# Kernel tuning notes

Measured on AMD Instinct MI355X. Metric: run time of the kernel, lower is better.

Reference implementation:

```python
import jax, jax.numpy as jnp
import numpy as np

HIDDEN = 768
NUM_LABELS = 25


def setup_inputs() -> dict:
    key = jax.random.key(0)
    k1, k2, k3, k4, k5 = jax.random.split(key, 5)
    B, H, S, E = 2, 12, 256, 64
    attention_probs = jax.random.uniform(k1, (B, H, S, S), dtype=jnp.float32)
    value_attentions = jax.random.normal(k2, (B, H, S, E), dtype=jnp.float32)
    relative_positions = jax.random.normal(k3, (B, S, S, H * E), dtype=jnp.float32)
    # nn.Linear(hidden_size, num_labels): weight [L, hidden], bias [L]
    bound = 1.0 / np.sqrt(HIDDEN)
    W = jax.random.uniform(k4, (NUM_LABELS, HIDDEN), dtype=jnp.float32, minval=-bound, maxval=bound)
    b = jax.random.uniform(k5, (NUM_LABELS,), dtype=jnp.float32, minval=-bound, maxval=bound)
    return {
        "attention_probs": attention_probs,
        "value_attentions": value_attentions,
        "relative_positions": relative_positions,
        "W": W,
        "b": b,
    }


def reference(attention_probs, value_attentions, relative_positions, W, b):
    B, H, S, E = value_attentions.shape
    # out[b,h,i,j,e] = probs[b,h,i,j] * (value[b,h,j,e] + rel[b,h,i,j,e])
    p = attention_probs[..., None]                      # [B,H,S,S,1]
    v = value_attentions[:, :, None, :, :]              # [B,H,1,S,E] broadcast over i
    rel = relative_positions.reshape(B, S, S, H, E).transpose(0, 3, 1, 2, 4)  # [B,H,S,S,E]
    out = p * (v + rel)                                 # [B,H,i,j,E]
    # permute(0,3,2,1,4) -> [B, j, i, H, E] -> [B,S,S,H*E]
    out = out.transpose(0, 3, 2, 1, 4).reshape(B, S, S, H * E)
    out = out @ W.T + b                                 # [B,S,S,L]
    return out.transpose(0, 1, 3, 2)                    # [B,S,L,S]
```

## Files before the change

kernel.cpp:

```cpp
#include <hip/hip_runtime.h>
#include <hip/hip_bf16.h>

#define NB 2
#define NH 12
#define NS 256
#define NE 64
#define NC 768
#define NL 25

#define CH 128
#define NCH 6
#define TI 128
#define SAS 132

typedef __attribute__((ext_vector_type(8))) short short8;
typedef __attribute__((ext_vector_type(4))) float float4v;

__device__ __forceinline__ unsigned short bfb(float x) {
    __hip_bfloat16 h = __float2bfloat16(x);
    return *reinterpret_cast<unsigned short*>(&h);
}
__device__ __forceinline__ unsigned int pk2(float x, float y) {
    return (unsigned int)bfb(x) | ((unsigned int)bfb(y) << 16);
}

__global__ void prep_w(const float* __restrict__ W, unsigned short* __restrict__ Wb) {
    int idx = blockIdx.x * 256 + threadIdx.x;
    if (idx >= 32 * NC) return;
    int row = idx / NC;
    int col = idx - row * NC;
    Wb[idx] = (row < NL) ? bfb(W[row * NC + col]) : (unsigned short)0;
}

__global__ __launch_bounds__(256, 4) void tmhs_mfma(
    const float* __restrict__ p,
    const float* __restrict__ v,
    const float* __restrict__ rel,
    const unsigned short* __restrict__ Wb,
    const float* __restrict__ bias,
    float* __restrict__ out)
{
    __shared__ unsigned short sA[TI][SAS];

    const int tid = threadIdx.x;
    const int bx  = blockIdx.x;
    const int ih  = bx & 1;
    const int j   = (bx >> 1) & 255;
    const int b   = bx >> 9;
    const int i0  = ih * TI;

    const int lane = tid & 63;
    const int wv   = tid >> 6;
    const int n15  = lane & 15;
    const int quad = lane >> 4;

    float4v z = {0.f, 0.f, 0.f, 0.f};
    float4v acc[2][2] = {{z, z}, {z, z}};

    const int srow  = tid >> 1;
    const int shalf = tid & 1;

    for (int ch = 0; ch < NCH; ++ch) {
        const int kc = ch * CH;
        const int h  = (kc >> 6) + shalf;
        __syncthreads();
        {
            const float  pr = p[((b*NH + h)*NS + (i0 + srow))*NS + j];
            const float4* rs = (const float4*)(rel + ((b*NS + i0 + srow)*NS + j)*NC + kc + shalf*64);
            const float4* vs = (const float4*)(v + ((b*NH + h)*NS + j)*NE);
            unsigned int* dst = (unsigned int*)&sA[srow][shalf*64];
#pragma unroll
            for (int q = 0; q < 16; ++q) {
                const float4 rr = rs[q];
                const float4 vv = vs[q];
                uint2 w2;
                w2.x = pk2(pr*(rr.x+vv.x), pr*(rr.y+vv.y));
                w2.y = pk2(pr*(rr.z+vv.z), pr*(rr.w+vv.w));
                *(uint2*)(dst + q*2) = w2;
            }
        }
        __syncthreads();

#pragma unroll
        for (int ks = 0; ks < 4; ++ks) {
            short8 af0 = *(const short8*)(Wb + (     n15)*NC + kc + ks*32 + quad*8);
            short8 af1 = *(const short8*)(Wb + (16 + n15)*NC + kc + ks*32 + quad*8);
#pragma unroll
            for (int nt = 0; nt < 2; ++nt) {
                const unsigned short* bp = &sA[wv*32 + nt*16 + n15][ks*32 + quad*8];
                union { short8 s8; unsigned long long d[2]; } bu;
                bu.d[0] = *(const unsigned long long*)bp;
                bu.d[1] = *(const unsigned long long*)(bp + 4);
                acc[0][nt] = __builtin_amdgcn_mfma_f32_16x16x32_bf16(af0, bu.s8, acc[0][nt], 0, 0, 0);
                acc[1][nt] = __builtin_amdgcn_mfma_f32_16x16x32_bf16(af1, bu.s8, acc[1][nt], 0, 0, 0);
            }
        }
    }

    const int obase = ((b*NS + j)*NL)*NS;
#pragma unroll
    for (int nt = 0; nt < 2; ++nt) {
        const int ii = i0 + wv*32 + nt*16 + n15;
#pragma unroll
        for (int mt = 0; mt < 2; ++mt) {
#pragma unroll
            for (int r = 0; r < 4; ++r) {
                const int l = mt*16 + quad*4 + r;
                if (l < NL)
                    out[obase + l*NS + ii] = acc[mt][nt][r] + bias[l];
            }
        }
    }
}

extern "C" void kernel_launch(void* const* d_in, const int* in_sizes, int n_in,
                              void* d_out, int out_size, void* d_ws, size_t ws_size,
                              hipStream_t stream) {
    const float* p    = (const float*)d_in[0];
    const float* v    = (const float*)d_in[1];
    const float* rel  = (const float*)d_in[2];
    const float* W    = (const float*)d_in[3];
    const float* bias = (const float*)d_in[4];
    float* out = (float*)d_out;
    unsigned short* Wb = (unsigned short*)d_ws;

    prep_w<<<dim3((32*NC + 255)/256), dim3(256), 0, stream>>>(W, Wb);
    tmhs_mfma<<<dim3(NB * NS * 2), dim3(256), 0, stream>>>(p, v, rel, Wb, bias, out);
}
```

Before: 560.1 us.

## Double-buffer rel via async global-to-LDS loads and fuse elementwise into MFMA operand build

Staging of the raw fp32 rel tile now uses global_load_lds into double-buffered shared memory, prefetching the next channel chunk while the current one is computed. The p*(rel+v) combination and bf16 packing move to the MFMA operand load, with per-row p values held in registers. Tiles shrink to 64 rows, doubling the grid, and launch bounds drop to 2 blocks per SM. The aim is to overlap the dominant rel memory traffic with compute and remove the separate convert-and-store pass. In exchange it uses more LDS per block, lowers occupancy, and re-reads v from global inside the inner loop.

```diff
diff --git a/kernel.cpp b/kernel.cpp
--- a/kernel.cpp
+++ b/kernel.cpp
@@ -10,8 +10,8 @@
 
 #define CH 128
 #define NCH 6
-#define TI 128
-#define SAS 132
+#define TI 64
+#define PAIRB 1040
 
 typedef __attribute__((ext_vector_type(8))) short short8;
 typedef __attribute__((ext_vector_type(4))) float float4v;
@@ -32,7 +32,7 @@
     Wb[idx] = (row < NL) ? bfb(W[row * NC + col]) : (unsigned short)0;
 }
 
-__global__ __launch_bounds__(256, 4) void tmhs_mfma(
+__global__ __launch_bounds__(256, 2) void tmhs_mfma(
     const float* __restrict__ p,
     const float* __restrict__ v,
     const float* __restrict__ rel,
@@ -40,75 +40,96 @@
     const float* __restrict__ bias,
     float* __restrict__ out)
 {
-    __shared__ unsigned short sA[TI][SAS];
+    __shared__ __align__(16) unsigned char sF[2][32 * PAIRB];
 
     const int tid = threadIdx.x;
     const int bx  = blockIdx.x;
-    const int ih  = bx & 1;
-    const int j   = (bx >> 1) & 255;
-    const int b   = bx >> 9;
-    const int i0  = ih * TI;
+    const int j   = bx & 255;
+    const int iq  = (bx >> 8) & 3;
+    const int b   = bx >> 10;
+    const int i0  = iq * TI;
 
     const int lane = tid & 63;
     const int wv   = tid >> 6;
     const int n15  = lane & 15;
     const int quad = lane >> 4;
+    const int l32  = lane & 31;
+    const int rh   = lane >> 5;
+
+    const int icol = i0 + wv * 16 + n15;
+
+    float ph[NH];
+#pragma unroll
+    for (int h = 0; h < NH; ++h)
+        ph[h] = p[((size_t)(b * NH + h) * NS + icol) * NS + j];
 
     float4v z = {0.f, 0.f, 0.f, 0.f};
-    float4v acc[2][2] = {{z, z}, {z, z}};
+    float4v acc[2] = {z, z};
 
-    const int srow  = tid >> 1;
-    const int shalf = tid & 1;
+    const int irow  = wv * 16 + n15;
+    const int rbyte = (irow >> 1) * PAIRB + (irow & 1) * 512;
+    const int qbase = wv * 8;
 
+    auto stage = [&](int pb, int ch) {
+        const int kc = ch * CH;
+#pragma unroll
+        for (int s = 0; s < 8; ++s) {
+            const int q   = qbase + s;
+            const int row = i0 + q * 2 + rh;
+            const float* gp = rel + ((size_t)(b * NS + row) * NS + j) * NC + kc + l32 * 4;
+            __builtin_amdgcn_global_load_lds(
+                (const __attribute__((address_space(1))) void*)gp,
+                (__attribute__((address_space(3))) void*)(&sF[pb][q * PAIRB]),
+                16, 0, 0);
+        }
+    };
+
+    stage(0, 0);
+    __syncthreads();
+
+#pragma unroll
     for (int ch = 0; ch < NCH; ++ch) {
         const int kc = ch * CH;
-        const int h  = (kc >> 6) + shalf;
-        __syncthreads();
-        {
-            const float  pr = p[((b*NH + h)*NS + (i0 + srow))*NS + j];
-            const float4* rs = (const float4*)(rel + ((b*NS + i0 + srow)*NS + j)*NC + kc + shalf*64);
-            const float4* vs = (const float4*)(v + ((b*NH + h)*NS + j)*NE);
-            unsigned int* dst = (unsigned int*)&sA[srow][shalf*64];
-#pragma unroll
-            for (int q = 0; q < 16; ++q) {
-                const float4 rr = rs[q];
-                const float4 vv = vs[q];
-                uint2 w2;
-                w2.x = pk2(pr*(rr.x+vv.x), pr*(rr.y+vv.y));
-                w2.y = pk2(pr*(rr.z+vv.z), pr*(rr.w+vv.w));
-                *(uint2*)(dst + q*2) = w2;
-            }
-        }
-        __syncthreads();
+        const int pb = ch & 1;
+
+        if (ch + 1 < NCH)
+            stage((ch + 1) & 1, ch + 1);
 
 #pragma unroll
         for (int ks = 0; ks < 4; ++ks) {
-            short8 af0 = *(const short8*)(Wb + (     n15)*NC + kc + ks*32 + quad*8);
-            short8 af1 = *(const short8*)(Wb + (16 + n15)*NC + kc + ks*32 + quad*8);
-#pragma unroll
-            for (int nt = 0; nt < 2; ++nt) {
-                const unsigned short* bp = &sA[wv*32 + nt*16 + n15][ks*32 + quad*8];
-                union { short8 s8; unsigned long long d[2]; } bu;
-                bu.d[0] = *(const unsigned long long*)bp;
-                bu.d[1] = *(const unsigned long long*)(bp + 4);
-                acc[0][nt] = __builtin_amdgcn_mfma_f32_16x16x32_bf16(af0, bu.s8, acc[0][nt], 0, 0, 0);
-                acc[1][nt] = __builtin_amdgcn_mfma_f32_16x16x32_bf16(af1, bu.s8, acc[1][nt], 0, 0, 0);
-            }
+            short8 af0 = *(const short8*)(Wb + (     n15) * NC + kc + ks * 32 + quad * 8);
+            short8 af1 = *(const short8*)(Wb + (16 + n15) * NC + kc + ks * 32 + quad * 8);
+
+            const unsigned char* bp = &sF[pb][rbyte + ks * 128 + quad * 32];
+            const float4 f0 = *(const float4*)bp;
+            const float4 f1 = *(const float4*)(bp + 16);
+            const float* vp = v + ((size_t)(b * NH + 2 * ch + (ks >> 1)) * NS + j) * NE
+                              + (ks & 1) * 32 + quad * 8;
+            const float4 v0 = *(const float4*)vp;
+            const float4 v1 = *(const float4*)(vp + 4);
+            const float  pr = ph[2 * ch + (ks >> 1)];
+
+            union { short8 s8; unsigned int u[4]; } bf;
+            bf.u[0] = pk2(pr * (f0.x + v0.x), pr * (f0.y + v0.y));
+            bf.u[1] = pk2(pr * (f0.z + v0.z), pr * (f0.w + v0.w));
+            bf.u[2] = pk2(pr * (f1.x + v1.x), pr * (f1.y + v1.y));
+            bf.u[3] = pk2(pr * (f1.z + v1.z), pr * (f1.w + v1.w));
+
+            acc[0] = __builtin_amdgcn_mfma_f32_16x16x32_bf16(af0, bf.s8, acc[0], 0, 0, 0);
+            acc[1] = __builtin_amdgcn_mfma_f32_16x16x32_bf16(af1, bf.s8, acc[1], 0, 0, 0);
         }
+
+        __syncthreads();
     }
 
-    const int obase = ((b*NS + j)*NL)*NS;
+    const size_t obase = ((size_t)(b * NS + j) * NL) * NS;
 #pragma unroll
-    for (int nt = 0; nt < 2; ++nt) {
-        const int ii = i0 + wv*32 + nt*16 + n15;
+    for (int mt = 0; mt < 2; ++mt) {
 #pragma unroll
-        for (int mt = 0; mt < 2; ++mt) {
-#pragma unroll
-            for (int r = 0; r < 4; ++r) {
-                const int l = mt*16 + quad*4 + r;
-                if (l < NL)
-                    out[obase + l*NS + ii] = acc[mt][nt][r] + bias[l];
-            }
+        for (int r = 0; r < 4; ++r) {
+            const int l = mt * 16 + quad * 4 + r;
+            if (l < NL)
+                out[obase + l * NS + icol] = acc[mt][r] + bias[l];
         }
     }
 }
@@ -124,6 +145,6 @@
     float* out = (float*)d_out;
     unsigned short* Wb = (unsigned short*)d_ws;
 
-    prep_w<<<dim3((32*NC + 255)/256), dim3(256), 0, stream>>>(W, Wb);
-    tmhs_mfma<<<dim3(NB * NS * 2), dim3(256), 0, stream>>>(p, v, rel, Wb, bias, out);
+    prep_w<<<dim3((32 * NC + 255) / 256), dim3(256), 0, stream>>>(W, Wb);
+    tmhs_mfma<<<dim3(NB * 4 * NS), dim3(256), 0, stream>>>(p, v, rel, Wb, bias, out);
 }
```

New measurement: 554.3 us. Within noise of the previous version (-1.0%).
